# Kernel optimization log

Measured on AMD Instinct MI355X. Metric: run time of the kernel, lower is better.

The kernel has to match this reference:

```python
import jax, jax.numpy as jnp
import numpy as np

D_MODEL = 1024
D_INNER = 2048
D_STATE = 16
D_CONV = 4
DT_RANK = 64  # ceil(D_MODEL / 16)
BATCH = 2
SEQLEN = 2048


def setup_inputs() -> dict:
    key = jax.random.key(0)
    ks = jax.random.split(key, 9)
    s = 0.02
    hidden_states = jax.random.normal(ks[0], (BATCH, SEQLEN, D_MODEL), dtype=jnp.float32)
    W_in = jax.random.normal(ks[1], (D_MODEL, 2 * D_INNER), dtype=jnp.float32) * s
    # flax depthwise Conv kernel layout: (window, in_features//groups=1, out_features)
    conv_kernel = jax.random.normal(ks[2], (D_CONV, 1, D_INNER), dtype=jnp.float32) * 0.2
    conv_bias = jax.random.normal(ks[3], (D_INNER,), dtype=jnp.float32) * s
    W_x = jax.random.normal(ks[4], (D_INNER, DT_RANK + 2 * D_STATE), dtype=jnp.float32) * s
    W_dt = jax.random.normal(ks[5], (DT_RANK, D_INNER), dtype=jnp.float32) * s
    b_dt = jax.random.normal(ks[6], (D_INNER,), dtype=jnp.float32) * s
    # A_log = log(arange(1, d_state+1)) broadcast over d_inner (constant init in module)
    A_log = jnp.log(jnp.broadcast_to(jnp.arange(1, D_STATE + 1, dtype=jnp.float32), (D_INNER, D_STATE)))
    D = jnp.ones((D_INNER,), dtype=jnp.float32)
    W_out = jax.random.normal(ks[7], (D_INNER, D_MODEL), dtype=jnp.float32) * s
    return {
        "hidden_states": hidden_states,
        "W_in": W_in,
        "conv_kernel": conv_kernel,
        "conv_bias": conv_bias,
        "W_x": W_x,
        "W_dt": W_dt,
        "b_dt": b_dt,
        "A_log": A_log,
        "D": D,
        "W_out": W_out,
    }


def _mamba_forward(hidden_states, W_in, conv_kernel, conv_bias, W_x, W_dt, b_dt, A_log, D, W_out):
    # in_proj, then einops '(d i)' split with i=2 => interleaved channels
    xz = hidden_states @ W_in                       # (b, l, 2*d_inner)
    x = xz[..., 0::2]                               # (b, l, d_inner)
    z = xz[..., 1::2]                               # (b, l, d_inner)

    # depthwise conv1d, padding='SAME' (as in flax nn.Conv)
    x = jax.lax.conv_general_dilated(
        x, conv_kernel, window_strides=(1,), padding="SAME",
        dimension_numbers=("NWC", "WIO", "NWC"),
        feature_group_count=D_INNER,
    ) + conv_bias
    x = jax.nn.silu(x)

    x_dbl = x @ W_x                                 # (b, l, dt_rank + 2*d_state)
    dt = x_dbl[..., :DT_RANK] @ W_dt + b_dt         # (b, l, d_inner)
    Bm = x_dbl[..., DT_RANK:DT_RANK + D_STATE]      # (b, l, n)
    Cm = x_dbl[..., DT_RANK + D_STATE:]             # (b, l, n)

    A = -jnp.exp(A_log.astype(jnp.float32))         # (d_inner, n)
    delta = jax.nn.softplus(dt.astype(jnp.float32)) # (b, l, d_inner)

    deltaA = jnp.exp(jnp.einsum("bld,dn->lbdn", delta, A))          # (l, b, d, n)
    deltaB_u = jnp.einsum("bld,bln,bld->lbdn", delta, Bm, x)        # (l, b, d, n)
    C_l = jnp.transpose(Cm, (1, 0, 2))                               # (l, b, n)

    state0 = jnp.zeros((BATCH, D_INNER, D_STATE), dtype=jnp.float32)

    def step(state, inputs):
        dA, dBu, c = inputs
        state = dA * state + dBu                    # (b, d, n)
        y = jnp.einsum("bdn,bn->bd", state, c)      # (b, d)
        return state, y

    _, y = jax.lax.scan(step, state0, (deltaA, deltaB_u, C_l))
    y = jnp.transpose(y, (1, 0, 2))                 # (b, l, d_inner)

    out = (y + x * D) * jax.nn.silu(z)              # skip via D, gate via silu(z)
    return out @ W_out                              # (b, l, d_model)


def reference(hidden_states, W_in, conv_kernel, conv_bias, W_x, W_dt, b_dt, A_log, D, W_out):
    return _mamba_forward(hidden_states, W_in, conv_kernel, conv_bias, W_x, W_dt, b_dt, A_log, D, W_out)
```

## Files before the change

kernel.cpp:

```cpp
#include <hip/hip_runtime.h>
#include <hip/hip_bf16.h>

typedef unsigned short u16;
typedef __attribute__((ext_vector_type(8))) short short8;
typedef __attribute__((ext_vector_type(4))) short short4v;
typedef __attribute__((ext_vector_type(4))) float f32x4;
typedef __attribute__((ext_vector_type(4))) float float4v;
typedef __attribute__((ext_vector_type(2))) float f32x2;

#define DMODEL 1024
#define DI 2048
#define NST 16
#define RANK 64
#define BB 2
#define LL 2048
#define MM (BB*LL)
#define LC 32
#define NCH (LL/LC)

__device__ __forceinline__ float b2f(u16 v){ union{unsigned u; float f;}x; x.u=(unsigned)v<<16; return x.f; }
__device__ __forceinline__ u16 f2b(float f){
  union{unsigned u; float f;}x; x.f=f;
  unsigned r = x.u + 0x7FFFu + ((x.u>>16)&1u);
  return (u16)(r>>16);
}
__device__ __forceinline__ bool probe_bf(const u16* probe){ return probe[1] != 0; }
__device__ __forceinline__ float ldin(const void* p, size_t i, bool bf){
  return bf ? b2f(((const u16*)p)[i]) : ((const float*)p)[i];
}
__device__ __forceinline__ u16 ldb(const void* p, size_t i, bool bf){
  return bf ? ((const u16*)p)[i] : f2b(((const float*)p)[i]);
}
__device__ __forceinline__ void gl16(const u16* g, char* lds_wave_base){
  __builtin_amdgcn_global_load_lds((const __attribute__((address_space(1))) unsigned*)g,
                                   (__attribute__((address_space(3))) unsigned*)lds_wave_base, 16, 0, 0);
}

template<int EPI>
__global__ __launch_bounds__(512,2) void mgemm256_k(
    const u16* __restrict__ A, const u16* __restrict__ Bt,
    void* __restrict__ O0, void* __restrict__ O1,
    int M, int N, int K, int lda, int ldb, int ldc)
{
  __shared__ char smem[131072];
  const int t = threadIdx.x;
  int bx = blockIdx.x, by = blockIdx.y;
  {
    const int gx = gridDim.x;
    const int nwg = gx*gridDim.y;
    const int lin = by*gx + bx;
    const int swz = (lin & 7)*(nwg>>3) + (lin>>3);
    bx = swz % gx; by = swz / gx;
  }
  const int m0 = by*256, n0 = bx*256;
  const int kbeg = blockIdx.z * K;
  const int wv = t >> 6, ln = t & 63;
  const int wr = wv >> 2, wc = wv & 3;
  const int lr = ln & 15, q = ln >> 4;
  const int NT = K >> 6;

  const int srow = ln >> 3;
  const int koff = ((ln & 7) ^ srow) * 8;
  const u16* AgP[4]; const u16* BgP[4];
#pragma unroll
  for(int c=0;c<4;c++){
    AgP[c] = A + (size_t)(m0 + (c*8+wv)*8 + srow)*lda + kbeg + koff;
    BgP[c] = Bt + (size_t)(n0 + (c*8+wv)*8 + srow)*ldb + kbeg + koff;
  }

  const int ck = ((q ^ (ln & 7)) * 16);
  int aro[8], bro[4];
#pragma unroll
  for(int i=0;i<8;i++) aro[i] = (wr*128 + i*16 + lr)*128 + ck;
#pragma unroll
  for(int j=0;j<4;j++) bro[j] = (wc*64 + j*16 + lr)*128 + ck;

  f32x4 acc[8][4];
#pragma unroll
  for(int i=0;i<8;i++)
#pragma unroll
    for(int j=0;j<4;j++) acc[i][j] = (f32x4){0.f,0.f,0.f,0.f};

  auto stage = [&](int kt, int cur){
    char* ab = smem + cur*65536;
    char* bb = ab + 32768;
#pragma unroll
    for(int c=0;c<4;c++) gl16(AgP[c] + kt*64, ab + (c*8+wv)*1024);
#pragma unroll
    for(int c=0;c<4;c++) gl16(BgP[c] + kt*64, bb + (c*8+wv)*1024);
  };

  stage(0,0);
  stage(1,1);

  for(int kt=0; kt<NT; ++kt){
    const int cur = kt & 1;
    if(kt == NT-1) asm volatile("s_waitcnt vmcnt(0)" ::: "memory");
    else           asm volatile("s_waitcnt vmcnt(8)" ::: "memory");
    __builtin_amdgcn_sched_barrier(0);
    __builtin_amdgcn_s_barrier();
    __builtin_amdgcn_sched_barrier(0);
    const char* ab = smem + cur*65536;
    const char* bb = ab + 32768;
    short8 afr[4], bfr[4];
#pragma unroll
    for(int j=0;j<4;j++) bfr[j] = *(const short8*)(bb + bro[j]);
#pragma unroll
    for(int i=0;i<4;i++) afr[i] = *(const short8*)(ab + aro[i]);
    __builtin_amdgcn_s_setprio(1);
#pragma unroll
    for(int i=0;i<4;i++)
#pragma unroll
      for(int j=0;j<4;j++)
        acc[i][j] = __builtin_amdgcn_mfma_f32_16x16x32_bf16(afr[i], bfr[j], acc[i][j], 0,0,0);
    __builtin_amdgcn_s_setprio(0);
#pragma unroll
    for(int i=0;i<4;i++) afr[i] = *(const short8*)(ab + aro[4+i]);
    __builtin_amdgcn_s_setprio(1);
#pragma unroll
    for(int i=0;i<4;i++)
#pragma unroll
      for(int j=0;j<4;j++)
        acc[4+i][j] = __builtin_amdgcn_mfma_f32_16x16x32_bf16(afr[i], bfr[j], acc[4+i][j], 0,0,0);
    __builtin_amdgcn_s_setprio(0);
#pragma unroll
    for(int j=0;j<4;j++) bfr[j] = *(const short8*)(bb + (bro[j]^64));
#pragma unroll
    for(int i=0;i<4;i++) afr[i] = *(const short8*)(ab + (aro[i]^64));
    __builtin_amdgcn_s_setprio(1);
#pragma unroll
    for(int i=0;i<4;i++)
#pragma unroll
      for(int j=0;j<4;j++)
        acc[i][j] = __builtin_amdgcn_mfma_f32_16x16x32_bf16(afr[i], bfr[j], acc[i][j], 0,0,0);
    __builtin_amdgcn_s_setprio(0);
#pragma unroll
    for(int i=0;i<4;i++) afr[i] = *(const short8*)(ab + (aro[4+i]^64));
    asm volatile("s_waitcnt lgkmcnt(0)" ::: "memory");
    __builtin_amdgcn_sched_barrier(0);
    __builtin_amdgcn_s_barrier();
    __builtin_amdgcn_sched_barrier(0);
    if(kt+2 < NT) stage(kt+2, cur);
    __builtin_amdgcn_sched_barrier(0);
    __builtin_amdgcn_s_setprio(1);
#pragma unroll
    for(int i=0;i<4;i++)
#pragma unroll
      for(int j=0;j<4;j++)
        acc[4+i][j] = __builtin_amdgcn_mfma_f32_16x16x32_bf16(afr[i], bfr[j], acc[4+i][j], 0,0,0);
    __builtin_amdgcn_s_setprio(0);
  }

  if(EPI==4){
    u16* tile = (u16*)smem;
    u16* obase = (n0 < DI) ? (u16*)O0 : (u16*)O1;
    const int cb = n0 & (DI-1);
    for(int h=0;h<2;h++){
      __builtin_amdgcn_s_barrier();
      if(wr == h){
#pragma unroll
        for(int i=0;i<8;i++)
#pragma unroll
          for(int r=0;r<4;r++){
            int trow = i*16 + q*4 + r;
#pragma unroll
            for(int j=0;j<4;j++)
              tile[trow*264 + wc*64 + j*16 + lr] = f2b(acc[i][j][r]);
          }
      }
      asm volatile("s_waitcnt lgkmcnt(0)" ::: "memory");
      __builtin_amdgcn_sched_barrier(0);
      __builtin_amdgcn_s_barrier();
      __builtin_amdgcn_sched_barrier(0);
#pragma unroll
      for(int it=0;it<8;it++){
        int idx = it*512 + t;
        int row = idx >> 5;
        int ch  = (idx & 31) * 8;
        short8 v = *(const short8*)(tile + row*264 + ch);
        *(short8*)(obase + (size_t)(m0 + h*128 + row)*ldc + cb + ch) = v;
      }
    }
    return;
  }
#pragma unroll
  for(int i=0;i<8;i++){
#pragma unroll
    for(int r=0;r<4;r++){
      int row = m0 + wr*128 + i*16 + q*4 + r;
#pragma unroll
      for(int j=0;j<4;j++){
        int col = n0 + wc*64 + j*16 + lr;
        ((float*)O0)[(size_t)blockIdx.z*M*ldc + (size_t)row*ldc + col] = acc[i][j][r];
      }
    }
  }
}

template<int EPI>
__global__ __launch_bounds__(256,2) void mgemm_k(
    const u16* __restrict__ A, const u16* __restrict__ Bt,
    void* __restrict__ O0, void* __restrict__ O1,
    const void* __restrict__ bias, const u16* __restrict__ probe,
    int M, int N, int K, int lda, int ldb, int ldc)
{
  __shared__ char smem[16384];
  const int t = threadIdx.x;
  int bx = blockIdx.x, by = blockIdx.y;
  {
    const int gx = gridDim.x;
    const int nwg = gx*gridDim.y;
    const int lin = by*gx + bx;
    const int swz = (lin & 7)*(nwg>>3) + (lin>>3);
    bx = swz % gx; by = swz / gx;
  }
  const int m0 = by*128, n0 = bx*128;
  const int kbeg = blockIdx.z * K;
  const int lane = t & 63;
  const int wv = t >> 6;
  const int wm = (wv>>1)*64, wn = (wv&1)*64;
  const int lr = lane & 15, q = lane >> 4;

  const int r0 = t>>2, q0 = t&3;
  const u16* Ag0 = A + kbeg + (size_t)(m0 + r0)*lda + q0*8;
  const u16* Ag1 = A + kbeg + (size_t)(m0 + 64 + r0)*lda + q0*8;
  const u16* Bg0 = Bt + kbeg + (size_t)(n0 + r0)*ldb + q0*8;
  const u16* Bg1 = Bt + kbeg + (size_t)(n0 + 64 + r0)*ldb + q0*8;
  char* const wbase = smem + (t & ~63)*16;
  char* const lA0 = wbase;
  char* const lA1 = wbase + 4096;
  char* const lB0 = wbase + 8192;
  char* const lB1 = wbase + 12288;

  int aro[4], bro[4];
#pragma unroll
  for(int i=0;i<4;i++) aro[i] = (wm + i*16 + lr)*64 + q*16;
#pragma unroll
  for(int j=0;j<4;j++) bro[j] = (wn + j*16 + lr)*64 + q*16;

  f32x4 acc[4][4];
#pragma unroll
  for(int i=0;i<4;i++)
#pragma unroll
    for(int j=0;j<4;j++) acc[i][j] = (f32x4){0.f,0.f,0.f,0.f};

  for(int k0=0;k0<K;k0+=32){
    __syncthreads();
    gl16(Ag0 + k0, lA0); gl16(Ag1 + k0, lA1);
    gl16(Bg0 + k0, lB0); gl16(Bg1 + k0, lB1);
    __syncthreads();
    short8 af[4], bfv[4];
#pragma unroll
    for(int i=0;i<4;i++) af[i] = *(const short8*)(smem + aro[i]);
#pragma unroll
    for(int j=0;j<4;j++) bfv[j] = *(const short8*)(smem + 8192 + bro[j]);
#pragma unroll
    for(int i=0;i<4;i++)
#pragma unroll
      for(int j=0;j<4;j++)
        acc[i][j] = __builtin_amdgcn_mfma_f32_16x16x32_bf16(af[i], bfv[j], acc[i][j], 0,0,0);
  }

#pragma unroll
  for(int i=0;i<4;i++){
#pragma unroll
    for(int r=0;r<4;r++){
      int row = m0 + wm + i*16 + q*4 + r;
#pragma unroll
      for(int j=0;j<4;j++){
        int col = n0 + wn + j*16 + lr;
        ((float*)O0)[(size_t)blockIdx.z*M*ldc + (size_t)row*ldc + col] = acc[i][j][r];
      }
    }
  }
}

__global__ __launch_bounds__(256,2) void dt_k(
    const u16* __restrict__ A,
    const u16* __restrict__ Bt,
    u16* __restrict__ O,
    const void* __restrict__ bias, const u16* __restrict__ probe)
{
  const bool bf = probe_bf(probe);
  __shared__ char smem[33792];
  const int t = threadIdx.x;
  int bx = blockIdx.x, by = blockIdx.y;
  {
    const int gx = gridDim.x;
    const int nwg = gx*gridDim.y;
    const int lin = by*gx + bx;
    const int swz = (lin & 7)*(nwg>>3) + (lin>>3);
    bx = swz % gx; by = swz / gx;
  }
  const int m0 = by*128, n0 = bx*128;
  const int lane = t & 63, wv = t >> 6;
  const int wm = (wv>>1)*64, wn = (wv&1)*64;
  const int lr = lane & 15, q = lane >> 4;

  const int srow = t >> 3;
  const int koff = (((t&7) ^ (srow&7)) * 8);
  const u16* gA = A  + (size_t)(m0 + srow)*128 + koff;
  const u16* gB = Bt + (size_t)(n0 + srow)*64  + koff;
  char* const lA = smem + wv*1024;
  char* const lB = smem + 16384 + wv*1024;
#pragma unroll
  for(int r=0;r<4;r++){
    gl16(gA + (size_t)r*32*128, lA + r*4096);
    gl16(gB + (size_t)r*32*64,  lB + r*4096);
  }
  __syncthreads();

  f32x4 acc[4][4];
#pragma unroll
  for(int i=0;i<4;i++)
#pragma unroll
    for(int j=0;j<4;j++) acc[i][j] = (f32x4){0.f,0.f,0.f,0.f};

#pragma unroll
  for(int ks=0;ks<2;ks++){
    short8 af[4], bfv[4];
#pragma unroll
    for(int i=0;i<4;i++){
      int row = wm + i*16 + lr;
      af[i] = *(const short8*)(smem + row*128 + (((ks*4+q) ^ (row&7))*16));
    }
#pragma unroll
    for(int j=0;j<4;j++){
      int row = wn + j*16 + lr;
      bfv[j] = *(const short8*)(smem + 16384 + row*128 + (((ks*4+q) ^ (row&7))*16));
    }
#pragma unroll
    for(int i=0;i<4;i++)
#pragma unroll
      for(int j=0;j<4;j++)
        acc[i][j] = __builtin_amdgcn_mfma_f32_16x16x32_bf16(af[i], bfv[j], acc[i][j], 0,0,0);
  }

  float bj[4];
#pragma unroll
  for(int j=0;j<4;j++) bj[j] = ldin(bias, n0 + wn + j*16 + lr, bf);
  __syncthreads();
  u16* tile = (u16*)smem;
#pragma unroll
  for(int i=0;i<4;i++)
#pragma unroll
    for(int r=0;r<4;r++){
      int trow = wm + i*16 + q*4 + r;
#pragma unroll
      for(int j=0;j<4;j++){
        int tcol = wn + j*16 + lr;
        float s = acc[i][j][r] + bj[j];
        float e = __expf(-fabsf(s));
        float sp = fmaxf(s, 0.f) + __logf(1.f + e);
        tile[trow*132 + tcol] = f2b(sp);
      }
    }
  __syncthreads();
#pragma unroll
  for(int it=0;it<8;it++){
    int idx = it*256 + t;
    int row = idx >> 4;
    int colc = (idx & 15) * 8;
    short8 v = *(const short8*)(tile + row*132 + colc);
    *(short8*)(O + (size_t)(m0+row)*DI + n0 + colc) = v;
  }
}

__device__ __forceinline__ void tr_block(
    const void* src, u16* dst, int R, int C, int bx, int by, bool bf, bool perm,
    int tid, u16 (*tile)[33])
{
  const int c0 = bx*32, r0 = by*32;
  const int tc = tid & 31, tr0 = tid >> 5;
#pragma unroll
  for(int i=0;i<4;i++){
    int r = tr0 + i*8;
    int gc = c0 + tc;
    tile[r][tc] = (gc < C) ? ldb(src, (size_t)(r0+r)*C + gc, bf) : (u16)0;
  }
  __syncthreads();
#pragma unroll
  for(int i=0;i<4;i++){
    int dr = c0 + tr0 + i*8;
    if(perm) dr = (dr>>1) + ((dr&1)<<11);
    int dc = r0 + tc;
    dst[(size_t)dr*R + dc] = tile[tc][tr0 + i*8];
  }
}

__global__ __launch_bounds__(256) void prep_k(
    const void* __restrict__ W_in, const void* __restrict__ W_out,
    const void* __restrict__ W_x, const void* __restrict__ W_dt,
    const void* __restrict__ hidden,
    u16* __restrict__ WinT, u16* __restrict__ WoutT, u16* __restrict__ WxT,
    u16* __restrict__ WdtT, u16* __restrict__ hb, const u16* __restrict__ probe)
{
  const bool bf = probe_bf(probe);
  __shared__ u16 tile[32][33];
  const int bid = blockIdx.x, t = threadIdx.x;
  if(bid < 4096){
    tr_block(W_in, WinT, DMODEL, 2*DI, bid & 127, bid >> 7, bf, true, t, tile);
  } else if(bid < 6144){
    int b2 = bid - 4096; tr_block(W_out, WoutT, DI, DMODEL, b2 & 31, b2 >> 5, bf, false, t, tile);
  } else if(bid < 6400){
    int b2 = bid - 6144; tr_block(W_x, WxT, DI, 96, b2 & 3, b2 >> 2, bf, false, t, tile);
  } else if(bid < 6528){
    int b2 = bid - 6400; tr_block(W_dt, WdtT, RANK, DI, b2 & 63, b2 >> 6, bf, false, t, tile);
  } else {
    size_t i = ((size_t)(bid - 6528)*256 + t)*8;
    if(bf){
      *(short8*)(hb+i) = *(const short8*)((const u16*)hidden + i);
    } else {
      float4v a = *(const float4v*)((const float*)hidden + i);
      float4v b = *(const float4v*)((const float*)hidden + i + 4);
      short8 r;
      r[0]=(short)f2b(a[0]); r[1]=(short)f2b(a[1]); r[2]=(short)f2b(a[2]); r[3]=(short)f2b(a[3]);
      r[4]=(short)f2b(b[0]); r[5]=(short)f2b(b[1]); r[6]=(short)f2b(b[2]); r[7]=(short)f2b(b[3]);
      *(short8*)(hb+i) = r;
    }
  }
}

__global__ __launch_bounds__(256) void redx_k(
    const float* __restrict__ P, float* __restrict__ xdbl, u16* __restrict__ xdblb)
{
  size_t i = ((size_t)blockIdx.x*256 + threadIdx.x)*4;
  float4v s = *(const float4v*)(P + i);
#pragma unroll
  for(int p=1;p<8;p++) s += *(const float4v*)(P + (size_t)p*MM*128 + i);
  *(float4v*)(xdbl + i) = s;
  short4v r; r[0]=(short)f2b(s[0]); r[1]=(short)f2b(s[1]); r[2]=(short)f2b(s[2]); r[3]=(short)f2b(s[3]);
  *(short4v*)(xdblb + i) = r;
}

__global__ __launch_bounds__(256) void red7_k(
    const float* __restrict__ P, void* __restrict__ out, const u16* __restrict__ probe)
{
  const bool bf = probe_bf(probe);
  size_t i = ((size_t)blockIdx.x*256 + threadIdx.x)*4;
  float4v s = *(const float4v*)(P + i);
#pragma unroll
  for(int p=1;p<4;p++) s += *(const float4v*)(P + (size_t)p*MM*DMODEL + i);
  if(bf){
    short4v r; r[0]=(short)f2b(s[0]); r[1]=(short)f2b(s[1]); r[2]=(short)f2b(s[2]); r[3]=(short)f2b(s[3]);
    *(short4v*)((u16*)out + i) = r;
  } else {
    *(float4v*)((float*)out + i) = s;
  }
}

__global__ __launch_bounds__(256) void conv_silu_k(
  const u16* __restrict__ xb, const void* __restrict__ w,
  const void* __restrict__ bias, u16* __restrict__ xcb,
  const u16* __restrict__ probe)
{
  const bool bf = probe_bf(probe);
  const int row = blockIdx.x;
  const int tt = row & (LL-1);
  const int d = threadIdx.x*8;
  float wv[4][8], bv[8];
  if(bf){
    short8 bb = *(const short8*)((const u16*)bias + d);
#pragma unroll
    for(int j=0;j<8;j++) bv[j] = b2f((u16)bb[j]);
#pragma unroll
    for(int k=0;k<4;k++){
      short8 ww = *(const short8*)((const u16*)w + k*DI + d);
#pragma unroll
      for(int j=0;j<8;j++) wv[k][j] = b2f((u16)ww[j]);
    }
  } else {
    *(float4v*)(bv)   = *(const float4v*)((const float*)bias + d);
    *(float4v*)(bv+4) = *(const float4v*)((const float*)bias + d + 4);
#pragma unroll
    for(int k=0;k<4;k++){
      *(float4v*)(wv[k])   = *(const float4v*)((const float*)w + k*DI + d);
      *(float4v*)(wv[k]+4) = *(const float4v*)((const float*)w + k*DI + d + 4);
    }
  }
  float acc[8];
#pragma unroll
  for(int j=0;j<8;j++) acc[j] = bv[j];
  const u16* xrow = xb + (size_t)row*DI + d;
#pragma unroll
  for(int k=0;k<4;k++){
    int o = tt - 1 + k;
    if(0<=o && o<LL){
      short8 xv = *(const short8*)(xrow + (ptrdiff_t)(k-1)*DI);
#pragma unroll
      for(int j=0;j<8;j++) acc[j] = fmaf(b2f((u16)xv[j]), wv[k][j], acc[j]);
    }
  }
  short8 sb;
#pragma unroll
  for(int j=0;j<8;j++){ float s = acc[j] / (1.f + __expf(-acc[j])); sb[j]=(short)f2b(s); }
  *(short8*)(xcb + (size_t)row*DI + d) = sb;
}

__global__ __launch_bounds__(256,4) void scan_a_k(
  const u16* __restrict__ dlb, const u16* __restrict__ xcb,
  const float* __restrict__ xdbl, const void* __restrict__ A_log,
  float* __restrict__ Bacc, float* __restrict__ sumdv,
  const u16* __restrict__ probe)
{
  const bool bf = probe_bf(probe);
  __shared__ float Bsh[LC][NST];
  const int t = threadIdx.x;
  const int d0 = blockIdx.x*256 + t;
  const int b = blockIdx.y, c = blockIdx.z;
  for(int i=t;i<LC*NST;i+=256){
    int l = i>>4, n = i&15;
    Bsh[l][n] = xdbl[((size_t)b*LL + (size_t)c*LC + l)*128 + 64 + n];
  }
  __syncthreads();
  float ac[NST], s[NST];
#pragma unroll
  for(int n=0;n<NST;n++){
    ac[n] = -__expf(ldin(A_log, (size_t)d0*NST+n, bf));
    s[n]=0.f;
  }
  bool geom = true;
  {
    float a0 = ac[0];
#pragma unroll
    for(int n=1;n<NST;n++) geom = geom && (fabsf(ac[n]-(n+1)*a0) <= 1e-4f*(n+1)*fabsf(a0));
  }
  float sum=0.f;
  const size_t base0 = ((size_t)b*LL + (size_t)c*LC)*DI + d0;
  const u16* dptr = dlb + base0;
  const u16* xptr = xcb + base0;

  auto stepA = [&](int l, u16 dp, u16 xp){
    float dv=b2f(dp), xv=b2f(xp);
    float du=dv*xv;
    sum+=dv;
    if(geom){
      float e=__expf(ac[0]*dv);
      float p=1.f;
#pragma unroll
      for(int n=0;n<NST;n++){
        p*=e; s[n]=fmaf(p, s[n], du*Bsh[l][n]);
      }
    } else {
#pragma unroll
      for(int n=0;n<NST;n++)
        s[n]=fmaf(__expf(ac[n]*dv), s[n], du*Bsh[l][n]);
    }
  };

  u16 dpA = dptr[0], xpA = xptr[0];
  u16 dpB = dptr[DI], xpB = xptr[DI];
  for(int l=0;l<LC;l+=2){
    int l2 = (l+2 < LC) ? l+2 : LC-1;
    int l3 = (l+3 < LC) ? l+3 : LC-1;
    u16 dpC = dptr[(size_t)l2*DI], xpC = xptr[(size_t)l2*DI];
    u16 dpD = dptr[(size_t)l3*DI], xpD = xptr[(size_t)l3*DI];
    stepA(l,   dpA, xpA);
    stepA(l+1, dpB, xpB);
    dpA=dpC; xpA=xpC; dpB=dpD; xpB=xpD;
  }

  const size_t ob = ((size_t)c*BB + b)*((size_t)NST*DI) + d0;
#pragma unroll
  for(int n=0;n<NST;n++) Bacc[ob + (size_t)n*DI] = s[n];
  sumdv[((size_t)c*BB + b)*DI + d0] = sum;
}

__global__ __launch_bounds__(256) void scan_b_k(
  const float* __restrict__ Bacc, const float* __restrict__ sumdv,
  const void* __restrict__ A_log, float* __restrict__ Sin,
  const u16* __restrict__ probe)
{
  const bool bf = probe_bf(probe);
  const int idx = blockIdx.x*256 + threadIdx.x;
  const int d = idx & (DI-1);
  const int n = (idx >> 11) & 15;
  const int b = idx >> 15;
  const float ac = -__expf(ldin(A_log, (size_t)d*NST+n, bf));
  float s = 0.f;
  float svN = sumdv[((size_t)0*BB + b)*DI + d];
  float bbN = Bacc[idx];
  for(int c=0;c<NCH;c++){
    int c1 = (c+1 < NCH) ? c+1 : NCH-1;
    float svC = sumdv[((size_t)c1*BB + b)*DI + d];
    float bbC = Bacc[(size_t)c1*((size_t)BB*NST*DI) + idx];
    float a = __expf(ac * svN);
    Sin[(size_t)c*((size_t)BB*NST*DI) + idx] = s;
    s = fmaf(a, s, bbN);
    svN = svC; bbN = bbC;
  }
}

__global__ __launch_bounds__(256,4) void scan_c_gate_k(
  const u16* __restrict__ dlb, const u16* __restrict__ xcb,
  const float* __restrict__ xdbl, const void* __restrict__ A_log,
  const float* __restrict__ Sin, const u16* __restrict__ zb,
  const void* __restrict__ Dw, u16* __restrict__ G,
  const u16* __restrict__ probe)
{
  const bool bf = probe_bf(probe);
  __shared__ float Bsh[LC][NST], Csh[LC][NST];
  const int t = threadIdx.x;
  const int d0 = blockIdx.x*256 + t;
  const int b = blockIdx.y, c = blockIdx.z;
  for(int i=t;i<LC*NST;i+=256){
    int l = i>>4, n = i&15;
    size_t ro = ((size_t)b*LL + (size_t)c*LC + l)*128;
    Bsh[l][n] = xdbl[ro + 64 + n];
    Csh[l][n] = xdbl[ro + 80 + n];
  }
  __syncthreads();
  float ac[NST], s[NST];
  const size_t ib = ((size_t)c*BB + b)*((size_t)NST*DI) + d0;
#pragma unroll
  for(int n=0;n<NST;n++)
    ac[n] = -__expf(ldin(A_log, (size_t)d0*NST+n, bf));
#pragma unroll
  for(int n=0;n<NST;n++) s[n] = Sin[ib + (size_t)n*DI];
  bool geom = true;
  {
    float a0 = ac[0];
#pragma unroll
    for(int n=1;n<NST;n++) geom = geom && (fabsf(ac[n]-(n+1)*a0) <= 1e-4f*(n+1)*fabsf(a0));
  }
  const float D0 = ldin(Dw, d0, bf);
  const size_t base0 = ((size_t)b*LL + (size_t)c*LC)*DI + d0;
  const u16* dptr = dlb + base0;
  const u16* xptr = xcb + base0;
  const u16* zptr = zb  + base0;

  auto stepC = [&](int l, u16 dp, u16 xp, u16 zz){
    float dv=b2f(dp), xv=b2f(xp);
    float du=dv*xv;
    float y=0.f;
    if(geom){
      float e=__expf(ac[0]*dv);
      float p=1.f;
#pragma unroll
      for(int n=0;n<NST;n++){
        p*=e; s[n]=fmaf(p, s[n], du*Bsh[l][n]); y=fmaf(s[n], Csh[l][n], y);
      }
    } else {
#pragma unroll
      for(int n=0;n<NST;n++){
        s[n]=fmaf(__expf(ac[n]*dv), s[n], du*Bsh[l][n]); y=fmaf(s[n], Csh[l][n], y);
      }
    }
    float z0 = b2f(zz);
    float g0 = z0 / (1.f + __expf(-z0));
    float o0 = (y + xv*D0) * g0;
    G[base0 + (size_t)l*DI] = f2b(o0);
  };

  u16 dpA = dptr[0], xpA = xptr[0], zzA = zptr[0];
  u16 dpB = dptr[DI], xpB = xptr[DI], zzB = zptr[DI];
  for(int l=0;l<LC;l+=2){
    int l2 = (l+2 < LC) ? l+2 : LC-1;
    int l3 = (l+3 < LC) ? l+3 : LC-1;
    u16 dpC = dptr[(size_t)l2*DI], xpC = xptr[(size_t)l2*DI], zzC = zptr[(size_t)l2*DI];
    u16 dpD = dptr[(size_t)l3*DI], xpD = xptr[(size_t)l3*DI], zzD = zptr[(size_t)l3*DI];
    stepC(l,   dpA, xpA, zzA);
    stepC(l+1, dpB, xpB, zzB);
    dpA=dpC; xpA=xpC; zzA=zzC; dpB=dpD; xpB=xpD; zzB=zzD;
  }
}

extern "C" void kernel_launch(void* const* d_in, const int* in_sizes, int n_in,
                              void* d_out, int out_size, void* d_ws, size_t ws_size,
                              hipStream_t stream)
{
  const void* hidden = d_in[0];
  const void* W_in   = d_in[1];
  const void* convw  = d_in[2];
  const void* convb  = d_in[3];
  const void* W_x    = d_in[4];
  const void* W_dt   = d_in[5];
  const void* b_dt   = d_in[6];
  const u16*  A_log  = (const u16*)d_in[7];
  const void* Dw     = d_in[8];
  const void* W_out  = d_in[9];

  char* p = (char*)d_ws;
  u16*   xb   = (u16*)  p;
  float* Sin  = (float*)p;
  float* Pw7  = (float*)p;
  u16*   zb   = (u16*)  (p + 16777216);
  u16*   xcb  = (u16*)  (p + 33554432);
  float* Bcc  = (float*)(p + 67108864);
  u16*   G    = (u16*)  (p + 83886080);
  float* Pw   = (float*)(p + 100663296);
  u16*   dlb  = (u16*)  (p + 100663296);
  u16*   hb   = (u16*)  (p + 117440512);
  float* sumdv= (float*)(p + 117440512);
  float* xdbl = (float*)(p + 134217728);
  u16*   xdblb= (u16*)  (p + 136314880);
  u16*   WinT = (u16*)  (p + 137363456);
  u16*   WoutT= (u16*)  (p + 145752064);
  u16*   WxT  = (u16*)  (p + 149946368);
  u16*   WdtT = (u16*)  (p + 150470656);

  prep_k<<<6528 + (MM*DMODEL)/(256*8), 256, 0, stream>>>(
      W_in, W_out, W_x, W_dt, hidden, WinT, WoutT, WxT, WdtT, hb, A_log);
  mgemm256_k<4><<<dim3(16,16), 512, 0, stream>>>(hb, WinT, xb, zb,
                                                 MM, 2*DI, DMODEL, DMODEL, DMODEL, DI);
  conv_silu_k<<<MM, 256, 0, stream>>>(xb, convw, convb, xcb, A_log);
  mgemm_k<1><<<dim3(1,32,8), 256, 0, stream>>>(xcb, WxT, Pw, nullptr, nullptr, A_log,
                                               MM, 128, DI/8, DI, DI, 128);
  redx_k<<<(MM*128)/(256*4), 256, 0, stream>>>(Pw, xdbl, xdblb);
  dt_k<<<dim3(16,32), 256, 0, stream>>>(xdblb, WdtT, dlb, b_dt, A_log);
  scan_a_k<<<dim3(DI/256, BB, NCH), 256, 0, stream>>>(dlb, xcb, xdbl, A_log, Bcc, sumdv, A_log);
  scan_b_k<<<(BB*NST*DI)/256, 256, 0, stream>>>(Bcc, sumdv, A_log, Sin, A_log);
  scan_c_gate_k<<<dim3(DI/256, BB, NCH), 256, 0, stream>>>(dlb, xcb, xdbl, A_log, Sin, zb, Dw, G, A_log);
  mgemm256_k<1><<<dim3(4,16,4), 512, 0, stream>>>(G, WoutT, Pw7, nullptr,
                                                  MM, DMODEL, DI/4, DI, DI, DMODEL);
  red7_k<<<(MM*DMODEL)/(256*4), 256, 0, stream>>>(Pw7, d_out, A_log);
}
```

Before: 285.8 us.

## Restructure big GEMM main loop into four-phase interleaved half-tile pipeline

Reworks the 256x256 bf16 MFMA GEMM so each K-step runs in four phases. Each phase loads one quarter of the operand fragments from LDS and issues a global-to-LDS load for the next tile halves, so global loads, LDS reads and MFMAs overlap more finely, in the style of HipKittens 8-wave ping-pong. The wave-to-tile mapping changes to interleaved 16-row/16-col subtiles spread across both halves, and both epilogues are updated to match. More barriers are added per iteration, and the vmcnt accounting for the in-flight loads has to be exactly right.

```diff
diff --git a/kernel.cpp b/kernel.cpp
--- a/kernel.cpp
+++ b/kernel.cpp
@@ -59,21 +59,28 @@
   const int lr = ln & 15, q = ln >> 4;
   const int NT = K >> 6;
 
-  const int srow = ln >> 3;
-  const int koff = ((ln & 7) ^ srow) * 8;
-  const u16* AgP[4]; const u16* BgP[4];
-#pragma unroll
-  for(int c=0;c<4;c++){
-    AgP[c] = A + (size_t)(m0 + (c*8+wv)*8 + srow)*lda + kbeg + koff;
-    BgP[c] = Bt + (size_t)(n0 + (c*8+wv)*8 + srow)*ldb + kbeg + koff;
-  }
-
-  const int ck = ((q ^ (ln & 7)) * 16);
-  int aro[8], bro[4];
-#pragma unroll
-  for(int i=0;i<8;i++) aro[i] = (wr*128 + i*16 + lr)*128 + ck;
-#pragma unroll
-  for(int j=0;j<4;j++) bro[j] = (wc*64 + j*16 + lr)*128 + ck;
+  const int srow8 = ln >> 3;
+  const int koff = ((ln & 7) ^ srow8) * 8;
+  auto stA = [&](int kt, int h){
+    char* d = smem + (kt&1)*65536 + h*16384;
+    const u16* g = A + (size_t)(m0 + h*128 + wv*8 + srow8)*lda + kbeg + kt*64 + koff;
+    gl16(g, d + wv*1024);
+    gl16(g + (size_t)64*lda, d + 8192 + wv*1024);
+  };
+  auto stB = [&](int kt, int h){
+    char* d = smem + (kt&1)*65536 + 32768 + h*16384;
+    const u16* g = Bt + (size_t)(n0 + h*128 + wv*8 + srow8)*ldb + kbeg + kt*64 + koff;
+    gl16(g, d + wv*1024);
+    gl16(g + (size_t)64*ldb, d + 8192 + wv*1024);
+  };
+
+  int arow[8], brow[4], ck[2];
+#pragma unroll
+  for(int s=0;s<8;s++)  arow[s] = (s>>2)*16384 + (wr*16 + (s&3)*32 + lr)*128;
+#pragma unroll
+  for(int s2=0;s2<4;s2++) brow[s2] = 32768 + (s2>>1)*16384 + (wc*16 + (s2&1)*64 + lr)*128;
+#pragma unroll
+  for(int ks=0;ks<2;ks++) ck[ks] = ((ks*4 + q) ^ (lr & 7)) * 16;
 
   f32x4 acc[8][4];
 #pragma unroll
@@ -81,74 +88,97 @@
 #pragma unroll
     for(int j=0;j<4;j++) acc[i][j] = (f32x4){0.f,0.f,0.f,0.f};
 
-  auto stage = [&](int kt, int cur){
-    char* ab = smem + cur*65536;
-    char* bb = ab + 32768;
-#pragma unroll
-    for(int c=0;c<4;c++) gl16(AgP[c] + kt*64, ab + (c*8+wv)*1024);
-#pragma unroll
-    for(int c=0;c<4;c++) gl16(BgP[c] + kt*64, bb + (c*8+wv)*1024);
-  };
-
-  stage(0,0);
-  stage(1,1);
-
+  stA(0,0); stB(0,0); stA(0,1); stB(0,1);
+  stA(1,0); stB(1,0);
+  asm volatile("s_waitcnt vmcnt(4)" ::: "memory");
+  __builtin_amdgcn_sched_barrier(0);
+  __builtin_amdgcn_s_barrier();
+  __builtin_amdgcn_sched_barrier(0);
+
+  short8 aR[4][2], b0R[2][2], b1R[2][2];
   for(int kt=0; kt<NT; ++kt){
-    const int cur = kt & 1;
-    if(kt == NT-1) asm volatile("s_waitcnt vmcnt(0)" ::: "memory");
-    else           asm volatile("s_waitcnt vmcnt(8)" ::: "memory");
-    __builtin_amdgcn_sched_barrier(0);
+    const char* base = smem + (kt&1)*65536;
+#pragma unroll
+    for(int s=0;s<4;s++)
+#pragma unroll
+      for(int ks=0;ks<2;ks++) aR[s][ks] = *(const short8*)(base + arow[s] + ck[ks]);
+#pragma unroll
+    for(int j=0;j<2;j++)
+#pragma unroll
+      for(int ks=0;ks<2;ks++) b0R[j][ks] = *(const short8*)(base + brow[j] + ck[ks]);
+    if(kt+1 < NT) stA(kt+1, 1);
     __builtin_amdgcn_s_barrier();
-    __builtin_amdgcn_sched_barrier(0);
-    const char* ab = smem + cur*65536;
-    const char* bb = ab + 32768;
-    short8 afr[4], bfr[4];
-#pragma unroll
-    for(int j=0;j<4;j++) bfr[j] = *(const short8*)(bb + bro[j]);
-#pragma unroll
-    for(int i=0;i<4;i++) afr[i] = *(const short8*)(ab + aro[i]);
+    asm volatile("s_waitcnt lgkmcnt(0)" ::: "memory");
+    __builtin_amdgcn_sched_barrier(0);
     __builtin_amdgcn_s_setprio(1);
 #pragma unroll
-    for(int i=0;i<4;i++)
-#pragma unroll
-      for(int j=0;j<4;j++)
-        acc[i][j] = __builtin_amdgcn_mfma_f32_16x16x32_bf16(afr[i], bfr[j], acc[i][j], 0,0,0);
+    for(int s=0;s<4;s++)
+#pragma unroll
+      for(int j=0;j<2;j++)
+#pragma unroll
+        for(int ks=0;ks<2;ks++)
+          acc[s][j] = __builtin_amdgcn_mfma_f32_16x16x32_bf16(aR[s][ks], b0R[j][ks], acc[s][j], 0,0,0);
     __builtin_amdgcn_s_setprio(0);
-#pragma unroll
-    for(int i=0;i<4;i++) afr[i] = *(const short8*)(ab + aro[4+i]);
+    __builtin_amdgcn_s_barrier();
+    __builtin_amdgcn_sched_barrier(0);
+#pragma unroll
+    for(int j=0;j<2;j++)
+#pragma unroll
+      for(int ks=0;ks<2;ks++) b1R[j][ks] = *(const short8*)(base + brow[2+j] + ck[ks]);
+    if(kt+1 < NT) stB(kt+1, 1);
+    __builtin_amdgcn_s_barrier();
+    asm volatile("s_waitcnt lgkmcnt(0)" ::: "memory");
+    __builtin_amdgcn_sched_barrier(0);
     __builtin_amdgcn_s_setprio(1);
 #pragma unroll
-    for(int i=0;i<4;i++)
-#pragma unroll
-      for(int j=0;j<4;j++)
-        acc[4+i][j] = __builtin_amdgcn_mfma_f32_16x16x32_bf16(afr[i], bfr[j], acc[4+i][j], 0,0,0);
+    for(int s=0;s<4;s++)
+#pragma unroll
+      for(int j=0;j<2;j++)
+#pragma unroll
+        for(int ks=0;ks<2;ks++)
+          acc[s][2+j] = __builtin_amdgcn_mfma_f32_16x16x32_bf16(aR[s][ks], b1R[j][ks], acc[s][2+j], 0,0,0);
     __builtin_amdgcn_s_setprio(0);
-#pragma unroll
-    for(int j=0;j<4;j++) bfr[j] = *(const short8*)(bb + (bro[j]^64));
-#pragma unroll
-    for(int i=0;i<4;i++) afr[i] = *(const short8*)(ab + (aro[i]^64));
+    __builtin_amdgcn_s_barrier();
+    __builtin_amdgcn_sched_barrier(0);
+#pragma unroll
+    for(int s=0;s<4;s++)
+#pragma unroll
+      for(int ks=0;ks<2;ks++) aR[s][ks] = *(const short8*)(base + arow[4+s] + ck[ks]);
+    if(kt+2 < NT) stA(kt+2, 0);
+    __builtin_amdgcn_s_barrier();
+    asm volatile("s_waitcnt lgkmcnt(0)" ::: "memory");
+    __builtin_amdgcn_sched_barrier(0);
     __builtin_amdgcn_s_setprio(1);
 #pragma unroll
-    for(int i=0;i<4;i++)
-#pragma unroll
-      for(int j=0;j<4;j++)
-        acc[i][j] = __builtin_amdgcn_mfma_f32_16x16x32_bf16(afr[i], bfr[j], acc[i][j], 0,0,0);
+    for(int s=0;s<4;s++)
+#pragma unroll
+      for(int j=0;j<2;j++)
+#pragma unroll
+        for(int ks=0;ks<2;ks++)
+          acc[4+s][j] = __builtin_amdgcn_mfma_f32_16x16x32_bf16(aR[s][ks], b0R[j][ks], acc[4+s][j], 0,0,0);
     __builtin_amdgcn_s_setprio(0);
-#pragma unroll
-    for(int i=0;i<4;i++) afr[i] = *(const short8*)(ab + (aro[4+i]^64));
-    asm volatile("s_waitcnt lgkmcnt(0)" ::: "memory");
-    __builtin_amdgcn_sched_barrier(0);
     __builtin_amdgcn_s_barrier();
     __builtin_amdgcn_sched_barrier(0);
-    if(kt+2 < NT) stage(kt+2, cur);
+    if(kt+2 < NT){
+      stB(kt+2, 0);
+      asm volatile("s_waitcnt vmcnt(4)" ::: "memory");
+    } else if(kt+1 < NT){
+      asm volatile("s_waitcnt vmcnt(0)" ::: "memory");
+    }
+    __builtin_amdgcn_sched_barrier(0);
+    __builtin_amdgcn_s_barrier();
     __builtin_amdgcn_sched_barrier(0);
     __builtin_amdgcn_s_setprio(1);
 #pragma unroll
-    for(int i=0;i<4;i++)
-#pragma unroll
-      for(int j=0;j<4;j++)
-        acc[4+i][j] = __builtin_amdgcn_mfma_f32_16x16x32_bf16(afr[i], bfr[j], acc[4+i][j], 0,0,0);
+    for(int s=0;s<4;s++)
+#pragma unroll
+      for(int j=0;j<2;j++)
+#pragma unroll
+        for(int ks=0;ks<2;ks++)
+          acc[4+s][2+j] = __builtin_amdgcn_mfma_f32_16x16x32_bf16(aR[s][ks], b1R[j][ks], acc[4+s][2+j], 0,0,0);
     __builtin_amdgcn_s_setprio(0);
+    __builtin_amdgcn_s_barrier();
+    __builtin_amdgcn_sched_barrier(0);
   }
 
   if(EPI==4){
@@ -157,17 +187,15 @@
     const int cb = n0 & (DI-1);
     for(int h=0;h<2;h++){
       __builtin_amdgcn_s_barrier();
-      if(wr == h){
-#pragma unroll
-        for(int i=0;i<8;i++)
-#pragma unroll
-          for(int r=0;r<4;r++){
-            int trow = i*16 + q*4 + r;
-#pragma unroll
-            for(int j=0;j<4;j++)
-              tile[trow*264 + wc*64 + j*16 + lr] = f2b(acc[i][j][r]);
-          }
-      }
+#pragma unroll
+      for(int s=0;s<4;s++)
+#pragma unroll
+        for(int r=0;r<4;r++){
+          int trow = wr*16 + s*32 + q*4 + r;
+#pragma unroll
+          for(int s2=0;s2<4;s2++)
+            tile[trow*264 + wc*16 + s2*64 + lr] = f2b(acc[h*4+s][s2][r]);
+        }
       asm volatile("s_waitcnt lgkmcnt(0)" ::: "memory");
       __builtin_amdgcn_sched_barrier(0);
       __builtin_amdgcn_s_barrier();
@@ -184,14 +212,14 @@
     return;
   }
 #pragma unroll
-  for(int i=0;i<8;i++){
+  for(int s=0;s<8;s++){
 #pragma unroll
     for(int r=0;r<4;r++){
-      int row = m0 + wr*128 + i*16 + q*4 + r;
-#pragma unroll
-      for(int j=0;j<4;j++){
-        int col = n0 + wc*64 + j*16 + lr;
-        ((float*)O0)[(size_t)blockIdx.z*M*ldc + (size_t)row*ldc + col] = acc[i][j][r];
+      int row = m0 + wr*16 + s*32 + q*4 + r;
+#pragma unroll
+      for(int s2=0;s2<4;s2++){
+        int col = n0 + wc*16 + s2*64 + lr;
+        ((float*)O0)[(size_t)blockIdx.z*M*ldc + (size_t)row*ldc + col] = acc[s][s2][r];
       }
     }
   }
```

Result: no change. 285.5 us (-0.1%).
